# Optimization experiments

Measured on AMD Instinct MI355X. Metric: run time of the kernel, lower is better.

The kernel has to match this reference:

```python
import jax, jax.numpy as jnp
import numpy as np

B, A, N_IN, N_POINTS = 64, 256, 512, 2048


def _sq_cdist(u, v):
    # |u_i - v_j|^2 via expansion, abs() as in the torch original
    d = -2.0 * (u @ v.T) + (u * u).sum(1)[:, None] + (v * v).sum(1)[None, :]
    return jnp.abs(d)


def setup_inputs() -> dict:
    key = jax.random.key(0)
    k1, k2, k3, k4 = jax.random.split(key, 4)
    x = jax.random.normal(k1, (B, A, N_IN), dtype=jnp.float32)
    atom_mask = jax.random.bernoulli(k2, 0.8, (B, A))  # ragged valid-atom mask
    inducing_points = jax.random.normal(k3, (N_POINTS, N_IN), dtype=jnp.float32)
    gamma = (1.0 + 0.25 * jax.random.normal(k4, (N_IN,), dtype=jnp.float32)) * np.sqrt(N_IN).astype(np.float32)
    return {"x": x, "atom_mask": atom_mask, "inducing_points": inducing_points, "gamma": gamma}


def reference(x, atom_mask, inducing_points, gamma):
    b, a, n_in = x.shape
    m = atom_mask.astype(x.dtype)                      # [B, A]
    mf = m[..., None]                                  # [B, A, 1]
    n = m.sum()
    # masked mean / unbiased std over valid atoms (torch .std is ddof=1)
    mean = (x * mf).sum((0, 1)) / n                    # [n_in]
    var = (((x - mean) ** 2) * mf).sum((0, 1)) / (n - 1.0)
    std = jnp.sqrt(var) + 1e-5                         # [n_in]
    xn = (x - mean) / std * mf                         # zero out padded atoms

    g2 = gamma ** 2 + 0.001                            # [n_in]
    z = (xn / g2).reshape(b * a, n_in)                 # [N, n_in]
    zi = inducing_points / g2                          # [M, n_in]

    Kx = jnp.exp(-_sq_cdist(z, zi))                    # [N, M]
    Kind = jnp.exp(-_sq_cdist(zi, zi))                 # [M, M]
    Kinv = jnp.linalg.inv(Kind + 0.05 * jnp.eye(Kind.shape[0], dtype=x.dtype))

    t = Kx @ Kinv                                      # [N, M]
    x_new = ((t @ inducing_points) * std + mean).reshape(b, a, n_in) * mf
    var_out = (1.0 - (t * Kx).sum(-1)).reshape(b, a) * m
    return x_new, var_out
```

## Files before the change

kernel.cpp:

```cpp
#include <hip/hip_runtime.h>
#include <math.h>
#include <stdint.h>

namespace {

constexpr int NROW = 16384;
constexpr int NF   = 512;
constexpr int MIND = 2048;
constexpr float CC = 0.98f;

typedef _Float16 half8 __attribute__((ext_vector_type(8)));
typedef float floatx4 __attribute__((ext_vector_type(4)));

__device__ __forceinline__ void gload16(const void* g, void* l) {
  __builtin_amdgcn_global_load_lds(
      (__attribute__((address_space(1))) void*)g,
      (__attribute__((address_space(3))) void*)l, 16, 0, 0);
}

__global__ __launch_bounds__(256) void stats_kernel(
    const float* __restrict__ x, const int* __restrict__ mask,
    float* __restrict__ sum, float* __restrict__ sumsq, float* __restrict__ cnt)
{
  const int t = threadIdx.x;
  const int row0 = blockIdx.x * 64;
  float s0 = 0.f, s1 = 0.f, q0 = 0.f, q1 = 0.f, c = 0.f;
  for (int r = 0; r < 64; ++r) {
    const int row = row0 + r;
    const float m = (mask[row] != 0) ? 1.f : 0.f;
    const float v0 = x[(size_t)row * NF + t];
    const float v1 = x[(size_t)row * NF + t + 256];
    s0 += m * v0; q0 += m * v0 * v0;
    s1 += m * v1; q1 += m * v1 * v1;
    c += m;
  }
  atomicAdd(&sum[t], s0);        atomicAdd(&sum[t + 256], s1);
  atomicAdd(&sumsq[t], q0);      atomicAdd(&sumsq[t + 256], q1);
  if (t == 0) atomicAdd(cnt, c);
}

__global__ __launch_bounds__(256) void finalize_stats(
    const float* __restrict__ sum, const float* __restrict__ sumsq,
    const float* __restrict__ cnt, const float* __restrict__ gamma,
    float* __restrict__ meanv, float* __restrict__ stdv,
    float* __restrict__ zsv, float* __restrict__ giv)
{
  const int f = blockIdx.x * 256 + threadIdx.x;
  const float n = cnt[0];
  const float mu = sum[f] / n;
  const float var = (sumsq[f] - sum[f] * mu) / (n - 1.0f);
  const float sd = sqrtf(var) + 1e-5f;
  const float g = gamma[f];
  const float g2 = g * g + 0.001f;
  meanv[f] = mu;
  stdv[f]  = sd;
  zsv[f]   = 1.0f / (sd * g2);
  giv[f]   = 1.0f / g2;
}

__global__ __launch_bounds__(256) void make_z(
    const float* __restrict__ x, const int* __restrict__ mask,
    const float* __restrict__ ip, const float* __restrict__ meanv,
    const float* __restrict__ zsv, const float* __restrict__ giv,
    _Float16* __restrict__ Zh, _Float16* __restrict__ Zih,
    float* __restrict__ rnorm, float* __restrict__ cnorm)
{
  const int row = blockIdx.x;
  const int t = threadIdx.x;
  float v0, v1;
  if (row < NROW) {
    const float m = (mask[row] != 0) ? 1.f : 0.f;
    v0 = (x[(size_t)row * NF + t      ] - meanv[t      ]) * zsv[t      ] * m;
    v1 = (x[(size_t)row * NF + t + 256] - meanv[t + 256]) * zsv[t + 256] * m;
    const _Float16 h0 = (_Float16)v0, h1 = (_Float16)v1;
    Zh[(size_t)row * NF + t] = h0;
    Zh[(size_t)row * NF + t + 256] = h1;
    v0 = (float)h0; v1 = (float)h1;
  } else {
    const int r = row - NROW;
    v0 = ip[(size_t)r * NF + t      ] * giv[t      ];
    v1 = ip[(size_t)r * NF + t + 256] * giv[t + 256];
    const _Float16 h0 = (_Float16)v0, h1 = (_Float16)v1;
    Zih[(size_t)r * NF + t] = h0;
    Zih[(size_t)r * NF + t + 256] = h1;
    v0 = (float)h0; v1 = (float)h1;
  }
  float nrm = v0 * v0 + v1 * v1;
  #pragma unroll
  for (int off = 32; off; off >>= 1) nrm += __shfl_xor(nrm, off);
  __shared__ float red[4];
  if ((t & 63) == 0) red[t >> 6] = nrm;
  __syncthreads();
  if (t == 0) {
    const float s = red[0] + red[1] + red[2] + red[3];
    if (row < NROW) rnorm[row] = s; else cnorm[row - NROW] = s;
  }
}

template <int EPI>
__global__ __launch_bounds__(256) void mfma_gemm(
    const _Float16* __restrict__ A, const _Float16* __restrict__ B,
    int M, int N, int K,
    const float* __restrict__ rn, const float* __restrict__ cn,
    _Float16* __restrict__ DKout, float* __restrict__ Cf,
    const _Float16* __restrict__ DK, const float* __restrict__ u,
    float* __restrict__ varacc,
    const float* __restrict__ colsumR,
    const float* __restrict__ stdv, const float* __restrict__ meanv,
    const int* __restrict__ mask)
{
  __shared__ __align__(16) _Float16 As[128 * 32];
  __shared__ __align__(16) _Float16 Bs[128 * 32];
  const int tid = threadIdx.x;
  const int w = tid >> 6, L = tid & 63;
  const int wm = w >> 1, wn = w & 1;
  const int bn = blockIdx.x, bm = blockIdx.y;
  const int lq = L >> 4;
  const int lr = L & 15;

  floatx4 acc[4][4] = {};

  const _Float16* Ag = A + (size_t)(bm * 128) * K;
  const _Float16* Bg = B + (size_t)(bn * 128) * K;
  const int srow = w * 32 + (L >> 2);
  const int scol = (L & 3) * 8;

  for (int k0 = 0; k0 < K; k0 += 32) {
    #pragma unroll
    for (int t = 0; t < 2; ++t) {
      const int r = srow + t * 16;
      gload16(Ag + (size_t)r * K + k0 + scol, As + r * 32 + scol);
      gload16(Bg + (size_t)r * K + k0 + scol, Bs + r * 32 + scol);
    }
    __syncthreads();
    half8 af[4], bf[4];
    #pragma unroll
    for (int mi = 0; mi < 4; ++mi)
      af[mi] = *(const half8*)&As[(wm * 64 + mi * 16 + lr) * 32 + lq * 8];
    #pragma unroll
    for (int ni = 0; ni < 4; ++ni)
      bf[ni] = *(const half8*)&Bs[(wn * 64 + ni * 16 + lr) * 32 + lq * 8];
    #pragma unroll
    for (int mi = 0; mi < 4; ++mi)
      #pragma unroll
      for (int ni = 0; ni < 4; ++ni)
        acc[mi][ni] = __builtin_amdgcn_mfma_f32_16x16x32_f16(
            af[mi], bf[ni], acc[mi][ni], 0, 0, 0);
    __syncthreads();
  }

  const int grb = bm * 128 + wm * 64;
  const int gcb = bn * 128 + wn * 64;

  if constexpr (EPI == 2) {
    #pragma unroll
    for (int mi = 0; mi < 4; ++mi)
      #pragma unroll
      for (int e = 0; e < 4; ++e) {
        const int gr = grb + mi * 16 + lq * 4 + e;
        float partial = 0.f;
        #pragma unroll
        for (int ni = 0; ni < 4; ++ni) {
          const int gc = gcb + ni * 16 + lr;
          const float t = acc[mi][ni][e] + CC * u[gc];
          const float kx = CC + (float)DK[(size_t)gr * N + gc];
          partial += t * kx;
        }
        partial += __shfl_xor(partial, 1);
        partial += __shfl_xor(partial, 2);
        partial += __shfl_xor(partial, 4);
        partial += __shfl_xor(partial, 8);
        if (lr == 0) atomicAdd(&varacc[gr], partial);
      }
  } else if constexpr (EPI == 3) {
    #pragma unroll
    for (int mi = 0; mi < 4; ++mi)
      #pragma unroll
      for (int e = 0; e < 4; ++e) {
        const int gr = grb + mi * 16 + lq * 4 + e;
        const float mrow = (mask[gr] != 0) ? 1.f : 0.f;
        #pragma unroll
        for (int ni = 0; ni < 4; ++ni) {
          const int gc = gcb + ni * 16 + lr;
          const float v = acc[mi][ni][e] + CC * colsumR[gc];
          Cf[(size_t)gr * N + gc] = (v * stdv[gc] + meanv[gc]) * mrow;
        }
      }
  } else {
    #pragma unroll
    for (int mi = 0; mi < 4; ++mi)
      #pragma unroll
      for (int e = 0; e < 4; ++e) {
        const int gr = grb + mi * 16 + lq * 4 + e;
        const float rni = rn[gr];
        #pragma unroll
        for (int ni = 0; ni < 4; ++ni) {
          const int gc = gcb + ni * 16 + lr;
          const float d = rni + cn[gc] - 2.f * acc[mi][ni][e];
          float kx = expf(-fabsf(d));
          if constexpr (EPI == 0) {
            DKout[(size_t)gr * N + gc] = (_Float16)(kx - CC);
          } else {
            if (gr == gc) kx += 0.05f;
            Cf[(size_t)gr * N + gc] = kx;
          }
        }
      }
  }
}

__global__ __launch_bounds__(256) void gemm_f32(
    const float* __restrict__ A, const float* __restrict__ B,
    float* __restrict__ C, int M, int N, int K)
{
  constexpr int BM = 64, BN = 64, BK = 16;
  const int tid = threadIdx.x;
  const int tx = tid % 16, ty = tid / 16;
  const int bn = blockIdx.x, bm = blockIdx.y;
  __shared__ float As[BK][BM + 4];
  __shared__ float Bs[BK][BN + 4];
  float acc[4][4] = {};
  const float* Ag = A + (size_t)bm * BM * K;
  const float* Bg = B + bn * BN;
  for (int k0 = 0; k0 < K; k0 += BK) {
    {
      const int r = tid >> 2, c4 = (tid & 3) << 2;
      const float4 av = *(const float4*)(Ag + (size_t)r * K + k0 + c4);
      As[c4 + 0][r] = av.x; As[c4 + 1][r] = av.y;
      As[c4 + 2][r] = av.z; As[c4 + 3][r] = av.w;
      const int kr = tid / 16, nc = (tid % 16) << 2;
      *(float4*)&Bs[kr][nc] = *(const float4*)(Bg + (size_t)(k0 + kr) * N + nc);
    }
    __syncthreads();
    #pragma unroll
    for (int kk = 0; kk < BK; ++kk) {
      const float4 a4 = *(const float4*)&As[kk][ty * 4];
      const float4 b4 = *(const float4*)&Bs[kk][tx * 4];
      const float a[4] = {a4.x, a4.y, a4.z, a4.w};
      const float b[4] = {b4.x, b4.y, b4.z, b4.w};
      #pragma unroll
      for (int i = 0; i < 4; ++i)
        #pragma unroll
        for (int j = 0; j < 4; ++j) acc[i][j] += a[i] * b[j];
    }
    __syncthreads();
  }
  #pragma unroll
  for (int i = 0; i < 4; ++i) {
    float4 o4; o4.x = acc[i][0]; o4.y = acc[i][1]; o4.z = acc[i][2]; o4.w = acc[i][3];
    *(float4*)(C + (size_t)(bm * BM + ty * 4 + i) * N + bn * BN + tx * 4) = o4;
  }
}


__global__ __launch_bounds__(256) void gj_diag(
    float* __restrict__ A, float* __restrict__ Pall, int k)
{
  const int o = k * 64;
  __shared__ float D[64][68];
  const int t = threadIdx.x;
  #pragma unroll
  for (int l = 0; l < 4; ++l) {
    const int v = t + l * 256;
    const int r = v >> 4, c4 = (v & 15) << 2;
    *(float4*)&D[r][c4] = *(const float4*)(A + (size_t)(o + r) * MIND + o + c4);
  }
  __syncthreads();
  const int i = t >> 2, c0 = (t & 3) * 16;
  for (int s = 0; s < 64; ++s) {
    const float p = 1.0f / D[s][s];
    if (t < 64 && t != s) D[s][t] *= p;
    __syncthreads();
    if (i != s) {
      const float f = D[i][s];
      #pragma unroll
      for (int c = c0; c < c0 + 16; c += 4) {
        float4 ds = *(const float4*)&D[s][c];
        float4 di = *(const float4*)&D[i][c];
        di.x -= f * ds.x; di.y -= f * ds.y; di.z -= f * ds.z; di.w -= f * ds.w;
        *(float4*)&D[i][c] = di;
      }
      if (s >= c0 && s < c0 + 16) D[i][s] = -f * p;
    }
    if (t == 0) D[s][s] = p;
    __syncthreads();
  }
  float* P = Pall + k * 4096;
  #pragma unroll
  for (int l = 0; l < 4; ++l) {
    const int v = t + l * 256;
    const int r = v >> 4, c4 = (v & 15) << 2;
    const float4 dv = *(const float4*)&D[r][c4];
    *(float4*)(P + r * 64 + c4) = dv;
    *(float4*)(A + (size_t)(o + r) * MIND + o + c4) = dv;
  }
}

__global__ __launch_bounds__(256) void gj_prep(
    const float* __restrict__ A, const float* __restrict__ Pall,
    float* __restrict__ CP, float* __restrict__ Bsave, int k)
{
  const int o = k * 64;
  const int t = threadIdx.x;
  if (blockIdx.x >= 32) {
    const int j0 = (blockIdx.x - 32) * 64;
    #pragma unroll
    for (int l = 0; l < 4; ++l) {
      const int v = t + l * 256;
      const int r = v >> 4, c4 = (v & 15) << 2;
      *(float4*)(Bsave + r * MIND + j0 + c4) =
          *(const float4*)(A + (size_t)(o + r) * MIND + j0 + c4);
    }
    return;
  }
  const int i0 = blockIdx.x * 64;
  if (i0 == o) return;
  const float* P = Pall + k * 4096;
  __shared__ float At[64][68];
  __shared__ float Pl[64][68];
  #pragma unroll
  for (int l = 0; l < 4; ++l) {
    const int v = t + l * 256;
    const int r = v >> 4, c4 = (v & 15) << 2;
    const float4 av = *(const float4*)(A + (size_t)(i0 + r) * MIND + o + c4);
    At[c4 + 0][r] = av.x; At[c4 + 1][r] = av.y;
    At[c4 + 2][r] = av.z; At[c4 + 3][r] = av.w;
    *(float4*)&Pl[r][c4] = *(const float4*)(P + r * 64 + c4);
  }
  __syncthreads();
  const int ty = t >> 4, tx = t & 15;
  float acc[4][4] = {};
  for (int s = 0; s < 64; ++s) {
    const float4 a4 = *(const float4*)&At[s][ty * 4];
    const float4 b4 = *(const float4*)&Pl[s][tx * 4];
    const float a[4] = {a4.x, a4.y, a4.z, a4.w};
    const float b[4] = {b4.x, b4.y, b4.z, b4.w};
    #pragma unroll
    for (int i = 0; i < 4; ++i)
      #pragma unroll
      for (int j = 0; j < 4; ++j) acc[i][j] += a[i] * b[j];
  }
  #pragma unroll
  for (int i = 0; i < 4; ++i) {
    float4 o4; o4.x = acc[i][0]; o4.y = acc[i][1]; o4.z = acc[i][2]; o4.w = acc[i][3];
    *(float4*)(CP + (i0 + ty * 4 + i) * 64 + tx * 4) = o4;
  }
}

__global__ __launch_bounds__(256) void gj_apply(
    float* __restrict__ A, float* __restrict__ Pall,
    const float* __restrict__ CP, const float* __restrict__ Bsave, int k)
{
  const int o = k * 64;
  const int i0 = blockIdx.y * 64, j0 = blockIdx.x * 64;
  const int t = threadIdx.x;

  if (i0 == o && j0 == o) return;

  if (j0 == o) {
    #pragma unroll
    for (int l = 0; l < 4; ++l) {
      const int v = t + l * 256;
      const int r = v >> 4, c4 = (v & 15) << 2;
      float4 x = *(const float4*)(CP + (i0 + r) * 64 + c4);
      x.x = -x.x; x.y = -x.y; x.z = -x.z; x.w = -x.w;
      *(float4*)(A + (size_t)(i0 + r) * MIND + o + c4) = x;
    }
    return;
  }

  __shared__ float S1[64 * 68];
  __shared__ float S2[64 * 68];
  #define DD(r, c) S1[(r) * 68 + (c)]

  const bool isrow = (i0 == o);
  const float* Lsrc = isrow ? (Pall + k * 4096) : (CP + i0 * 64);
  #pragma unroll
  for (int l = 0; l < 4; ++l) {
    const int v = t + l * 256;
    const int r = v >> 4, c4 = (v & 15) << 2;
    const float4 lv = *(const float4*)(Lsrc + r * 64 + c4);
    S1[(c4 + 0) * 68 + r] = lv.x; S1[(c4 + 1) * 68 + r] = lv.y;
    S1[(c4 + 2) * 68 + r] = lv.z; S1[(c4 + 3) * 68 + r] = lv.w;
    *(float4*)&S2[r * 68 + c4] = *(const float4*)(Bsave + r * MIND + j0 + c4);
  }
  __syncthreads();
  const int ty = t >> 4, tx = t & 15;
  float acc[4][4] = {};
  for (int s = 0; s < 64; ++s) {
    const float4 a4 = *(const float4*)&S1[s * 68 + ty * 4];
    const float4 b4 = *(const float4*)&S2[s * 68 + tx * 4];
    const float a[4] = {a4.x, a4.y, a4.z, a4.w};
    const float b[4] = {b4.x, b4.y, b4.z, b4.w};
    #pragma unroll
    for (int i = 0; i < 4; ++i)
      #pragma unroll
      for (int j = 0; j < 4; ++j) acc[i][j] += a[i] * b[j];
  }

  if (isrow) {
    #pragma unroll
    for (int i = 0; i < 4; ++i) {
      float4 o4; o4.x = acc[i][0]; o4.y = acc[i][1]; o4.z = acc[i][2]; o4.w = acc[i][3];
      *(float4*)(A + (size_t)(o + ty * 4 + i) * MIND + j0 + tx * 4) = o4;
    }
    return;
  }

  const bool isdiagnext = (i0 == o + 64) && (j0 == o + 64);
  if (!isdiagnext) {
    #pragma unroll
    for (int i = 0; i < 4; ++i) {
      float* cp = A + (size_t)(i0 + ty * 4 + i) * MIND + j0 + tx * 4;
      float4 cv = *(const float4*)cp;
      cv.x -= acc[i][0]; cv.y -= acc[i][1]; cv.z -= acc[i][2]; cv.w -= acc[i][3];
      *(float4*)cp = cv;
    }
    return;
  }

  __syncthreads();
  #pragma unroll
  for (int i = 0; i < 4; ++i) {
    const float4 cv = *(const float4*)(A + (size_t)(i0 + ty * 4 + i) * MIND + j0 + tx * 4);
    DD(ty * 4 + i, tx * 4 + 0) = cv.x - acc[i][0];
    DD(ty * 4 + i, tx * 4 + 1) = cv.y - acc[i][1];
    DD(ty * 4 + i, tx * 4 + 2) = cv.z - acc[i][2];
    DD(ty * 4 + i, tx * 4 + 3) = cv.w - acc[i][3];
  }
  __syncthreads();
  const int di = t >> 2, c0 = (t & 3) * 16;
  for (int s = 0; s < 64; ++s) {
    const float p = 1.0f / DD(s, s);
    if (t < 64 && t != s) DD(s, t) *= p;
    __syncthreads();
    if (di != s) {
      const float f = DD(di, s);
      #pragma unroll
      for (int c = c0; c < c0 + 16; c += 4) {
        float4 ds = *(const float4*)&DD(s, c);
        float4 dv = *(const float4*)&DD(di, c);
        dv.x -= f * ds.x; dv.y -= f * ds.y; dv.z -= f * ds.z; dv.w -= f * ds.w;
        *(float4*)&DD(di, c) = dv;
      }
      if (s >= c0 && s < c0 + 16) DD(di, s) = -f * p;
    }
    if (t == 0) DD(s, s) = p;
    __syncthreads();
  }
  float* Pn = Pall + (k + 1) * 4096;
  #pragma unroll
  for (int l = 0; l < 4; ++l) {
    const int v = t + l * 256;
    const int r = v >> 4, c4 = (v & 15) << 2;
    const float4 dv = *(const float4*)&DD(r, c4);
    *(float4*)(Pn + r * 64 + c4) = dv;
    *(float4*)(A + (size_t)(i0 + r) * MIND + j0 + c4) = dv;
  }
  #undef DD
}

__global__ __launch_bounds__(256) void rowsum_kernel(
    const float* __restrict__ Ai, float* __restrict__ u)
{
  const int row = blockIdx.x * 4 + (threadIdx.x >> 6);
  const int lane = threadIdx.x & 63;
  float s = 0.f;
  for (int c = lane; c < MIND; c += 64) s += Ai[(size_t)row * MIND + c];
  #pragma unroll
  for (int off = 32; off; off >>= 1) s += __shfl_xor(s, off);
  if (lane == 0) u[row] = s;
}

typedef _Float16 half4v __attribute__((ext_vector_type(4)));
__global__ __launch_bounds__(256) void cast_half4(
    const float* __restrict__ s, _Float16* __restrict__ d)
{
  const int i = (blockIdx.x * 256 + threadIdx.x) * 4;
  const float4 v = *(const float4*)(s + i);
  half4v h; h.x = (_Float16)v.x; h.y = (_Float16)v.y;
  h.z = (_Float16)v.z; h.w = (_Float16)v.w;
  *(half4v*)(d + i) = h;
}

__global__ __launch_bounds__(256) void transpose_cast(
    const float* __restrict__ R, _Float16* __restrict__ Rt)
{
  __shared__ float T[64][65];
  const int j0 = blockIdx.x * 64;
  const int f0 = blockIdx.y * 64;
  const int t = threadIdx.x;
  #pragma unroll
  for (int l = 0; l < 16; ++l) {
    const int idx = t + l * 256;
    T[idx >> 6][idx & 63] = R[(size_t)(j0 + (idx >> 6)) * NF + f0 + (idx & 63)];
  }
  __syncthreads();
  #pragma unroll
  for (int l = 0; l < 16; ++l) {
    const int idx = t + l * 256;
    const int fr = idx >> 6, jc = idx & 63;
    Rt[(size_t)(f0 + fr) * MIND + j0 + jc] = (_Float16)T[jc][fr];
  }
}

__global__ __launch_bounds__(256) void colsum_kernel(
    const float* __restrict__ R, float* __restrict__ cs)
{
  const int b = blockIdx.x;
  const int t = threadIdx.x;
  float s0 = 0.f, s1 = 0.f;
  for (int r = 0; r < 64; ++r) {
    s0 += R[(size_t)(b * 64 + r) * NF + t];
    s1 += R[(size_t)(b * 64 + r) * NF + t + 256];
  }
  atomicAdd(&cs[t], s0); atomicAdd(&cs[t + 256], s1);
}

__global__ __launch_bounds__(256) void var_finalize(
    const float* __restrict__ varacc, const int* __restrict__ mask,
    float* __restrict__ outv)
{
  const int i = blockIdx.x * 256 + threadIdx.x;
  const float m = (mask[i] != 0) ? 1.f : 0.f;
  outv[i] = (1.0f - varacc[i]) * m;
}

}

extern "C" void kernel_launch(void* const* d_in, const int* in_sizes, int n_in,
                              void* d_out, int out_size, void* d_ws, size_t ws_size,
                              hipStream_t stream)
{
  (void)in_sizes; (void)n_in; (void)out_size; (void)ws_size;
  const float* x     = (const float*)d_in[0];
  const int*   mask  = (const int*)d_in[1];
  const float* ip    = (const float*)d_in[2];
  const float* gamma = (const float*)d_in[3];
  float* out = (float*)d_out;

  float* w       = (float*)d_ws;
  float* sum     = w;
  float* sumsq   = w + 512;
  float* cnt     = w + 1024;
  float* varacc  = w + 1536;
  float* colsumR = w + 17920;
  float* meanv   = w + 18432;
  float* stdv    = w + 18944;
  float* zsv     = w + 19456;
  float* giv     = w + 19968;
  float* rnorm   = w + 20480;
  float* cnorm   = w + 36864;
  float* u       = w + 38912;
  float* Ai      = w + 40960;
  float* R       = w + 4235264;
  float* Pall    = w + 5283840;
  float* CP      = w + 5414912;
  float* Bsave   = w + 5545984;
  _Float16* hb   = (_Float16*)(w + 5677056);
  _Float16* Zh   = hb;
  _Float16* Zih  = hb + 8388608;
  _Float16* DK   = hb + 9437184;
  _Float16* Kih  = hb + 42991616;
  _Float16* Rt   = hb + 47185920;

  hipMemsetAsync(w, 0, 18432 * sizeof(float), stream);

  stats_kernel<<<256, 256, 0, stream>>>(x, mask, sum, sumsq, cnt);
  finalize_stats<<<2, 256, 0, stream>>>(sum, sumsq, cnt, gamma, meanv, stdv, zsv, giv);
  make_z<<<NROW + MIND, 256, 0, stream>>>(x, mask, ip, meanv, zsv, giv, Zh, Zih, rnorm, cnorm);

  mfma_gemm<0><<<dim3(MIND / 128, NROW / 128), 256, 0, stream>>>(
      Zh, Zih, NROW, MIND, NF, rnorm, cnorm,
      DK, nullptr, nullptr, nullptr, nullptr, nullptr, nullptr, nullptr, nullptr);
  mfma_gemm<1><<<dim3(MIND / 128, MIND / 128), 256, 0, stream>>>(
      Zih, Zih, MIND, MIND, NF, cnorm, cnorm,
      nullptr, Ai, nullptr, nullptr, nullptr, nullptr, nullptr, nullptr, nullptr);

  gj_diag<<<1, 256, 0, stream>>>(Ai, Pall, 0);
  gj_prep<<<64, 256, 0, stream>>>(Ai, Pall, CP, Bsave, 0);
  for (int k = 0; k < 32; ++k) {
    gj_apply<<<dim3(32, 32), 256, 0, stream>>>(Ai, Pall, CP, Bsave, k);
    if (k < 31) gj_prep<<<64, 256, 0, stream>>>(Ai, Pall, CP, Bsave, k + 1);
  }

  gemm_f32<<<dim3(NF / 64, MIND / 64), 256, 0, stream>>>(Ai, ip, R, MIND, NF, MIND);
  transpose_cast<<<dim3(MIND / 64, NF / 64), 256, 0, stream>>>(R, Rt);
  colsum_kernel<<<MIND / 64, 256, 0, stream>>>(R, colsumR);
  rowsum_kernel<<<MIND / 4, 256, 0, stream>>>(Ai, u);
  cast_half4<<<(MIND * MIND) / 1024, 256, 0, stream>>>(Ai, Kih);

  mfma_gemm<2><<<dim3(MIND / 128, NROW / 128), 256, 0, stream>>>(
      DK, Kih, NROW, MIND, MIND, nullptr, nullptr,
      nullptr, nullptr, DK, u, varacc, nullptr, nullptr, nullptr, nullptr);

  mfma_gemm<3><<<dim3(NF / 128, NROW / 128), 256, 0, stream>>>(
      DK, Rt, NROW, NF, MIND, nullptr, nullptr,
      nullptr, out, nullptr, nullptr, nullptr, colsumR, stdv, meanv, mask);

  var_finalize<<<NROW / 256, 256, 0, stream>>>(varacc, mask, out + (size_t)NROW * NF);
}
```

Baseline: 2.170 ms.

## Fuse blocked Gauss-Jordan inversion into one cooperative kernel with grid syncs

Replaces the roughly 65 separate gj_diag/gj_prep/gj_apply launches with a single cooperative kernel of 512 blocks. The kernel loops over the 32 pivot steps and separates phases with grid.sync(). Each block handles two tile jobs per step, and the next diagonal-pivot job is given to a block of its own so it is not stuck behind a second tile. The aim is to remove per-launch overhead and tail gaps between the many small dependent kernels. In exchange it relies on cooperative-launch residency and pays grid-wide barrier costs.

Measured after the change: 5.138 ms. +136.8%, slower.

```diff
diff --git a/kernel.cpp b/kernel.cpp
--- a/kernel.cpp
+++ b/kernel.cpp
@@ -1,6 +1,9 @@
 #include <hip/hip_runtime.h>
+#include <hip/hip_cooperative_groups.h>
 #include <math.h>
 #include <stdint.h>
+
+namespace cg = cooperative_groups;
 
 namespace {
 
@@ -253,128 +256,54 @@
 }
 
 
-__global__ __launch_bounds__(256) void gj_diag(
-    float* __restrict__ A, float* __restrict__ Pall, int k)
-{
+__device__ __forceinline__ void pivot64(float* D, int t)
+{
+  const int di = t >> 2, c0 = (t & 3) * 16;
+  for (int s = 0; s < 64; ++s) {
+    const float p = 1.0f / D[s * 68 + s];
+    if (t < 64 && t != s) D[s * 68 + t] *= p;
+    __syncthreads();
+    if (di != s) {
+      const float f = D[di * 68 + s];
+      #pragma unroll
+      for (int c = c0; c < c0 + 16; c += 4) {
+        float4 ds = *(const float4*)&D[s * 68 + c];
+        float4 dv = *(const float4*)&D[di * 68 + c];
+        dv.x -= f * ds.x; dv.y -= f * ds.y; dv.z -= f * ds.z; dv.w -= f * ds.w;
+        *(float4*)&D[di * 68 + c] = dv;
+      }
+      if (s >= c0 && s < c0 + 16) D[di * 68 + s] = -f * p;
+    }
+    if (t == 0) D[s * 68 + s] = p;
+    __syncthreads();
+  }
+}
+
+__device__ void apply_job(
+    float* __restrict__ A, float* __restrict__ Pall,
+    const float* __restrict__ CP, const float* __restrict__ Bsave,
+    int k, int job, int t, float* S1, float* S2)
+{
+  if (job < 0) return;
   const int o = k * 64;
-  __shared__ float D[64][68];
-  const int t = threadIdx.x;
-  #pragma unroll
-  for (int l = 0; l < 4; ++l) {
-    const int v = t + l * 256;
-    const int r = v >> 4, c4 = (v & 15) << 2;
-    *(float4*)&D[r][c4] = *(const float4*)(A + (size_t)(o + r) * MIND + o + c4);
-  }
-  __syncthreads();
-  const int i = t >> 2, c0 = (t & 3) * 16;
-  for (int s = 0; s < 64; ++s) {
-    const float p = 1.0f / D[s][s];
-    if (t < 64 && t != s) D[s][t] *= p;
-    __syncthreads();
-    if (i != s) {
-      const float f = D[i][s];
-      #pragma unroll
-      for (int c = c0; c < c0 + 16; c += 4) {
-        float4 ds = *(const float4*)&D[s][c];
-        float4 di = *(const float4*)&D[i][c];
-        di.x -= f * ds.x; di.y -= f * ds.y; di.z -= f * ds.z; di.w -= f * ds.w;
-        *(float4*)&D[i][c] = di;
-      }
-      if (s >= c0 && s < c0 + 16) D[i][s] = -f * p;
-    }
-    if (t == 0) D[s][s] = p;
-    __syncthreads();
-  }
-  float* P = Pall + k * 4096;
-  #pragma unroll
-  for (int l = 0; l < 4; ++l) {
-    const int v = t + l * 256;
-    const int r = v >> 4, c4 = (v & 15) << 2;
-    const float4 dv = *(const float4*)&D[r][c4];
-    *(float4*)(P + r * 64 + c4) = dv;
-    *(float4*)(A + (size_t)(o + r) * MIND + o + c4) = dv;
-  }
-}
-
-__global__ __launch_bounds__(256) void gj_prep(
-    const float* __restrict__ A, const float* __restrict__ Pall,
-    float* __restrict__ CP, float* __restrict__ Bsave, int k)
-{
-  const int o = k * 64;
-  const int t = threadIdx.x;
-  if (blockIdx.x >= 32) {
-    const int j0 = (blockIdx.x - 32) * 64;
+  const int i0 = (job >> 5) * 64, j0 = (job & 31) * 64;
+  if (i0 == o && j0 == o) return;
+
+  if (j0 == o) {
     #pragma unroll
     for (int l = 0; l < 4; ++l) {
       const int v = t + l * 256;
       const int r = v >> 4, c4 = (v & 15) << 2;
-      *(float4*)(Bsave + r * MIND + j0 + c4) =
-          *(const float4*)(A + (size_t)(o + r) * MIND + j0 + c4);
-    }
-    return;
-  }
-  const int i0 = blockIdx.x * 64;
-  if (i0 == o) return;
-  const float* P = Pall + k * 4096;
-  __shared__ float At[64][68];
-  __shared__ float Pl[64][68];
-  #pragma unroll
-  for (int l = 0; l < 4; ++l) {
-    const int v = t + l * 256;
-    const int r = v >> 4, c4 = (v & 15) << 2;
-    const float4 av = *(const float4*)(A + (size_t)(i0 + r) * MIND + o + c4);
-    At[c4 + 0][r] = av.x; At[c4 + 1][r] = av.y;
-    At[c4 + 2][r] = av.z; At[c4 + 3][r] = av.w;
-    *(float4*)&Pl[r][c4] = *(const float4*)(P + r * 64 + c4);
-  }
-  __syncthreads();
-  const int ty = t >> 4, tx = t & 15;
-  float acc[4][4] = {};
-  for (int s = 0; s < 64; ++s) {
-    const float4 a4 = *(const float4*)&At[s][ty * 4];
-    const float4 b4 = *(const float4*)&Pl[s][tx * 4];
-    const float a[4] = {a4.x, a4.y, a4.z, a4.w};
-    const float b[4] = {b4.x, b4.y, b4.z, b4.w};
-    #pragma unroll
-    for (int i = 0; i < 4; ++i)
-      #pragma unroll
-      for (int j = 0; j < 4; ++j) acc[i][j] += a[i] * b[j];
-  }
-  #pragma unroll
-  for (int i = 0; i < 4; ++i) {
-    float4 o4; o4.x = acc[i][0]; o4.y = acc[i][1]; o4.z = acc[i][2]; o4.w = acc[i][3];
-    *(float4*)(CP + (i0 + ty * 4 + i) * 64 + tx * 4) = o4;
-  }
-}
-
-__global__ __launch_bounds__(256) void gj_apply(
-    float* __restrict__ A, float* __restrict__ Pall,
-    const float* __restrict__ CP, const float* __restrict__ Bsave, int k)
-{
-  const int o = k * 64;
-  const int i0 = blockIdx.y * 64, j0 = blockIdx.x * 64;
-  const int t = threadIdx.x;
-
-  if (i0 == o && j0 == o) return;
-
-  if (j0 == o) {
-    #pragma unroll
-    for (int l = 0; l < 4; ++l) {
-      const int v = t + l * 256;
-      const int r = v >> 4, c4 = (v & 15) << 2;
-      float4 x = *(const float4*)(CP + (i0 + r) * 64 + c4);
+      float4 x = *(const float4*)(CP + (size_t)(i0 + r) * 64 + c4);
       x.x = -x.x; x.y = -x.y; x.z = -x.z; x.w = -x.w;
       *(float4*)(A + (size_t)(i0 + r) * MIND + o + c4) = x;
     }
     return;
   }
 
-  __shared__ float S1[64 * 68];
-  __shared__ float S2[64 * 68];
-  #define DD(r, c) S1[(r) * 68 + (c)]
-
+  __syncthreads();
   const bool isrow = (i0 == o);
-  const float* Lsrc = isrow ? (Pall + k * 4096) : (CP + i0 * 64);
+  const float* Lsrc = isrow ? (Pall + (size_t)k * 4096) : (CP + (size_t)i0 * 64);
   #pragma unroll
   for (int l = 0; l < 4; ++l) {
     const int v = t + l * 256;
@@ -382,7 +311,7 @@
     const float4 lv = *(const float4*)(Lsrc + r * 64 + c4);
     S1[(c4 + 0) * 68 + r] = lv.x; S1[(c4 + 1) * 68 + r] = lv.y;
     S1[(c4 + 2) * 68 + r] = lv.z; S1[(c4 + 3) * 68 + r] = lv.w;
-    *(float4*)&S2[r * 68 + c4] = *(const float4*)(Bsave + r * MIND + j0 + c4);
+    *(float4*)&S2[r * 68 + c4] = *(const float4*)(Bsave + (size_t)r * MIND + j0 + c4);
   }
   __syncthreads();
   const int ty = t >> 4, tx = t & 15;
@@ -407,8 +336,8 @@
     return;
   }
 
-  const bool isdiagnext = (i0 == o + 64) && (j0 == o + 64);
-  if (!isdiagnext) {
+  const bool isdiag = (k < 31) && (i0 == o + 64) && (j0 == o + 64);
+  if (!isdiag) {
     #pragma unroll
     for (int i = 0; i < 4; ++i) {
       float* cp = A + (size_t)(i0 + ty * 4 + i) * MIND + j0 + tx * 4;
@@ -423,41 +352,125 @@
   #pragma unroll
   for (int i = 0; i < 4; ++i) {
     const float4 cv = *(const float4*)(A + (size_t)(i0 + ty * 4 + i) * MIND + j0 + tx * 4);
-    DD(ty * 4 + i, tx * 4 + 0) = cv.x - acc[i][0];
-    DD(ty * 4 + i, tx * 4 + 1) = cv.y - acc[i][1];
-    DD(ty * 4 + i, tx * 4 + 2) = cv.z - acc[i][2];
-    DD(ty * 4 + i, tx * 4 + 3) = cv.w - acc[i][3];
-  }
-  __syncthreads();
-  const int di = t >> 2, c0 = (t & 3) * 16;
-  for (int s = 0; s < 64; ++s) {
-    const float p = 1.0f / DD(s, s);
-    if (t < 64 && t != s) DD(s, t) *= p;
-    __syncthreads();
-    if (di != s) {
-      const float f = DD(di, s);
-      #pragma unroll
-      for (int c = c0; c < c0 + 16; c += 4) {
-        float4 ds = *(const float4*)&DD(s, c);
-        float4 dv = *(const float4*)&DD(di, c);
-        dv.x -= f * ds.x; dv.y -= f * ds.y; dv.z -= f * ds.z; dv.w -= f * ds.w;
-        *(float4*)&DD(di, c) = dv;
-      }
-      if (s >= c0 && s < c0 + 16) DD(di, s) = -f * p;
-    }
-    if (t == 0) DD(s, s) = p;
-    __syncthreads();
-  }
-  float* Pn = Pall + (k + 1) * 4096;
+    S1[(ty * 4 + i) * 68 + tx * 4 + 0] = cv.x - acc[i][0];
+    S1[(ty * 4 + i) * 68 + tx * 4 + 1] = cv.y - acc[i][1];
+    S1[(ty * 4 + i) * 68 + tx * 4 + 2] = cv.z - acc[i][2];
+    S1[(ty * 4 + i) * 68 + tx * 4 + 3] = cv.w - acc[i][3];
+  }
+  __syncthreads();
+  pivot64(S1, t);
+  float* Pn = Pall + (size_t)(k + 1) * 4096;
   #pragma unroll
   for (int l = 0; l < 4; ++l) {
     const int v = t + l * 256;
     const int r = v >> 4, c4 = (v & 15) << 2;
-    const float4 dv = *(const float4*)&DD(r, c4);
+    const float4 dv = *(const float4*)&S1[r * 68 + c4];
     *(float4*)(Pn + r * 64 + c4) = dv;
     *(float4*)(A + (size_t)(i0 + r) * MIND + j0 + c4) = dv;
   }
-  #undef DD
+}
+
+__device__ void prep_job(
+    const float* __restrict__ A, const float* __restrict__ Pall,
+    float* __restrict__ CP, float* __restrict__ Bsave,
+    int k, int b, int t, float* S1, float* S2)
+{
+  const int o = k * 64;
+  if (b >= 64) return;
+  if (b >= 32) {
+    const int j0 = (b - 32) * 64;
+    #pragma unroll
+    for (int l = 0; l < 4; ++l) {
+      const int v = t + l * 256;
+      const int r = v >> 4, c4 = (v & 15) << 2;
+      *(float4*)(Bsave + (size_t)r * MIND + j0 + c4) =
+          *(const float4*)(A + (size_t)(o + r) * MIND + j0 + c4);
+    }
+    return;
+  }
+  const int i0 = b * 64;
+  if (i0 == o) return;
+  __syncthreads();
+  const float* P = Pall + (size_t)k * 4096;
+  #pragma unroll
+  for (int l = 0; l < 4; ++l) {
+    const int v = t + l * 256;
+    const int r = v >> 4, c4 = (v & 15) << 2;
+    const float4 av = *(const float4*)(A + (size_t)(i0 + r) * MIND + o + c4);
+    S1[(c4 + 0) * 68 + r] = av.x; S1[(c4 + 1) * 68 + r] = av.y;
+    S1[(c4 + 2) * 68 + r] = av.z; S1[(c4 + 3) * 68 + r] = av.w;
+    *(float4*)&S2[r * 68 + c4] = *(const float4*)(P + r * 64 + c4);
+  }
+  __syncthreads();
+  const int ty = t >> 4, tx = t & 15;
+  float acc[4][4] = {};
+  for (int s = 0; s < 64; ++s) {
+    const float4 a4 = *(const float4*)&S1[s * 68 + ty * 4];
+    const float4 b4 = *(const float4*)&S2[s * 68 + tx * 4];
+    const float a[4] = {a4.x, a4.y, a4.z, a4.w};
+    const float b[4] = {b4.x, b4.y, b4.z, b4.w};
+    #pragma unroll
+    for (int i = 0; i < 4; ++i)
+      #pragma unroll
+      for (int j = 0; j < 4; ++j) acc[i][j] += a[i] * b[j];
+  }
+  #pragma unroll
+  for (int i = 0; i < 4; ++i) {
+    float4 o4; o4.x = acc[i][0]; o4.y = acc[i][1]; o4.z = acc[i][2]; o4.w = acc[i][3];
+    *(float4*)(CP + (size_t)(i0 + ty * 4 + i) * 64 + tx * 4) = o4;
+  }
+}
+
+__global__ __launch_bounds__(256) void gj_coop(
+    float* __restrict__ A, float* __restrict__ Pall,
+    float* __restrict__ CP, float* __restrict__ Bsave)
+{
+  cg::grid_group grid = cg::this_grid();
+  const int b = blockIdx.x;
+  const int t = threadIdx.x;
+  __shared__ float S1[64 * 68];
+  __shared__ float S2[64 * 68];
+
+  if (b == 0) {
+    #pragma unroll
+    for (int l = 0; l < 4; ++l) {
+      const int v = t + l * 256;
+      const int r = v >> 4, c4 = (v & 15) << 2;
+      *(float4*)&S1[r * 68 + c4] = *(const float4*)(A + (size_t)r * MIND + c4);
+    }
+    __syncthreads();
+    pivot64(S1, t);
+    #pragma unroll
+    for (int l = 0; l < 4; ++l) {
+      const int v = t + l * 256;
+      const int r = v >> 4, c4 = (v & 15) << 2;
+      const float4 dv = *(const float4*)&S1[r * 68 + c4];
+      *(float4*)(Pall + r * 64 + c4) = dv;
+      *(float4*)(A + (size_t)r * MIND + c4) = dv;
+    }
+  }
+  grid.sync();
+  prep_job(A, Pall, CP, Bsave, 0, b, t, S1, S2);
+  grid.sync();
+
+  for (int k = 0; k < 32; ++k) {
+    int j1 = b, j2 = b + 512, j3 = -1;
+    if (k < 31) {
+      const int djob = 33 * (k + 1);
+      const int db = djob & 511;
+      const int sib = djob ^ 512;
+      if (b == db) { j1 = djob; j2 = -1; }
+      else if (b == ((db + 1) & 511)) { j3 = sib; }
+    }
+    apply_job(A, Pall, CP, Bsave, k, j1, t, S1, S2);
+    apply_job(A, Pall, CP, Bsave, k, j2, t, S1, S2);
+    apply_job(A, Pall, CP, Bsave, k, j3, t, S1, S2);
+    grid.sync();
+    if (k < 31) {
+      prep_job(A, Pall, CP, Bsave, k + 1, b, t, S1, S2);
+      grid.sync();
+    }
+  }
 }
 
 __global__ __launch_bounds__(256) void rowsum_kernel(
@@ -577,11 +590,9 @@
       Zih, Zih, MIND, MIND, NF, cnorm, cnorm,
       nullptr, Ai, nullptr, nullptr, nullptr, nullptr, nullptr, nullptr, nullptr);
 
-  gj_diag<<<1, 256, 0, stream>>>(Ai, Pall, 0);
-  gj_prep<<<64, 256, 0, stream>>>(Ai, Pall, CP, Bsave, 0);
-  for (int k = 0; k < 32; ++k) {
-    gj_apply<<<dim3(32, 32), 256, 0, stream>>>(Ai, Pall, CP, Bsave, k);
-    if (k < 31) gj_prep<<<64, 256, 0, stream>>>(Ai, Pall, CP, Bsave, k + 1);
+  {
+    void* args[] = {(void*)&Ai, (void*)&Pall, (void*)&CP, (void*)&Bsave};
+    hipLaunchCooperativeKernel((void*)gj_coop, dim3(512), dim3(256), args, 0, stream);
   }
 
   gemm_f32<<<dim3(NF / 64, MIND / 64), 256, 0, stream>>>(Ai, ip, R, MIND, NF, MIND);
```
